# Optimization experiments

Measured on AMD Instinct MI355X. Metric: run time of the kernel, lower is better.

## Reference

```python
import jax, jax.numpy as jnp
import numpy as np

B, L, E, H = 1, 2048, 1024, 16
HW = E // H  # head width = 64
SCALE = HW ** -0.5


def setup_inputs() -> dict:
    key = jax.random.key(0)
    ks = jax.random.split(key, 8)
    x = jax.random.normal(ks[0], (B, L, E), dtype=jnp.float32)
    mask = jax.random.bernoulli(ks[1], 0.9, (B, L))
    mask = mask.at[:, 0].set(True)  # guarantee at least one valid key per batch
    bias = jax.random.normal(ks[2], (B, L, L, H), dtype=jnp.float32)
    # torch nn.Linear stores weight as [out, in]; we keep that convention
    w_proj = jax.random.normal(ks[3], (3 * E, E), dtype=jnp.float32) * (E ** -0.5)
    w_o = jax.random.normal(ks[4], (E, E), dtype=jnp.float32) * (E ** -0.5)
    b_o = jax.random.normal(ks[5], (E,), dtype=jnp.float32) * 0.02
    w_g = jax.random.normal(ks[6], (E, E), dtype=jnp.float32) * (E ** -0.5)
    b_g = jax.random.normal(ks[7], (E,), dtype=jnp.float32) * 0.02
    return {"x": x, "mask": mask, "bias": bias, "w_proj": w_proj,
            "w_o": w_o, "b_o": b_o, "w_g": w_g, "b_g": b_g}


def reference(x, mask, bias, w_proj, w_o, b_o, w_g, b_g):
    # proj -> [B, L, 3E], rearrange '(h c)' with h=H so each head slice holds [q|k|v]
    t = jnp.einsum('ble,fe->blf', x, w_proj)               # [B, L, 3E]
    t = t.reshape(B, L, H, 3 * HW).transpose(0, 2, 1, 3)   # [B, H, L, 3*HW]
    q, k, v = jnp.split(t, 3, axis=-1)                     # each [B, H, L, HW]
    a = jnp.einsum('bhqc,bhkc->bhqk', SCALE * q, k)        # [B, H, L, L]
    a = a + bias.transpose(0, 3, 1, 2)                     # bias: [B,Lq,Lk,H] -> [B,H,Lq,Lk]
    a = jnp.where(mask[:, None, None, :], a, -jnp.inf)
    a = jax.nn.softmax(a, axis=-1)
    y = jnp.einsum('bhqk,bhkc->bqhc', a, v).reshape(B, L, E)
    g = jax.nn.sigmoid(jnp.einsum('ble,fe->blf', x, w_g) + b_g)
    y = g * y
    return jnp.einsum('ble,fe->blf', y, w_o) + b_o
```

## Files before the change

kernel.cpp:

```cpp
#include <hip/hip_runtime.h>
#include <stdint.h>

#define LSEQ 2048
#define EMB  1024
#define NH   16
#define HWID 64
#define SCALEF 0.125f

typedef __attribute__((ext_vector_type(4))) float  f32x4;
typedef __attribute__((ext_vector_type(8))) short  bf16x8;
typedef __attribute__((ext_vector_type(8))) unsigned short u16x8;
typedef __attribute__((ext_vector_type(4))) unsigned short u16x4;

static __device__ __forceinline__ unsigned short f2bf(float f) {
    union { float f; unsigned int u; } v; v.f = f;
    unsigned int r = (v.u + 0x7FFFu + ((v.u >> 16) & 1u)) >> 16;
    return (unsigned short)r;
}
static __device__ __forceinline__ float bf2f(unsigned short h) {
    union { unsigned int u; float f; } v; v.u = ((unsigned int)h) << 16;
    return v.f;
}

static __device__ __forceinline__ void gload_lds16(const void* g, void* l) {
    __builtin_amdgcn_global_load_lds((const __attribute__((address_space(1))) void*)g,
                                     (__attribute__((address_space(3))) void*)l,
                                     16, 0, 0);
}

__global__ __launch_bounds__(256) void convert_kernel(
    const float* __restrict__ x, const float* __restrict__ wp,
    const float* __restrict__ wg, const float* __restrict__ wo,
    unsigned short* __restrict__ xb, unsigned short* __restrict__ wcat,
    unsigned short* __restrict__ wob)
{
    const int NX  = (LSEQ * EMB) / 4;
    const int NWP = (3 * EMB * EMB) / 4;
    const int NWG = (EMB * EMB) / 4;
    const int NWO = (EMB * EMB) / 4;
    const int total = NX + NWP + NWG + NWO;
    for (int i = blockIdx.x * blockDim.x + threadIdx.x; i < total;
         i += gridDim.x * blockDim.x) {
        const float4* src; unsigned short* dst; int j;
        if (i < NX)                  { src = (const float4*)x;  dst = xb;                  j = i; }
        else if (i < NX + NWP)       { src = (const float4*)wp; dst = wcat;                j = i - NX; }
        else if (i < NX + NWP + NWG) { src = (const float4*)wg; dst = wcat + 3 * EMB * EMB; j = i - NX - NWP; }
        else                         { src = (const float4*)wo; dst = wob;                 j = i - NX - NWP - NWG; }
        float4 v = src[j];
        u16x4 o;
        o.x = f2bf(v.x); o.y = f2bf(v.y); o.z = f2bf(v.z); o.w = f2bf(v.w);
        *(u16x4*)(dst + (size_t)j * 4) = o;
    }
}

__global__ void decode_mask_kernel(const unsigned char* __restrict__ mask,
                                   unsigned char* __restrict__ valid)
{
    __shared__ int cnt;
    if (threadIdx.x == 0) cnt = 0;
    __syncthreads();
    int c = 0;
    for (int i = threadIdx.x; i < LSEQ; i += 256) c += (mask[i] != 0);
    atomicAdd(&cnt, c);
    __syncthreads();
    bool isbyte = cnt > LSEQ / 2;
    for (int k = threadIdx.x; k < LSEQ; k += 256) {
        unsigned char v;
        if (isbyte) v = (mask[k] != 0);
        else        v = ((mask[4*k] | mask[4*k+1] | mask[4*k+2] | mask[4*k+3]) != 0);
        valid[k] = v;
    }
}

#define BM 128
#define BN 128
#define BK 64

__global__ __launch_bounds__(256) void gemm_bt_kernel(
    const unsigned short* __restrict__ A, const unsigned short* __restrict__ B,
    void* __restrict__ Cout, const float* __restrict__ biasN,
    int M, int N, int K, int epi)
{
    __shared__ unsigned short As[BM][BK];
    __shared__ unsigned short Bs[BN][BK];
    const int tid  = threadIdx.x;
    const int lane = tid & 63;
    const int w    = tid >> 6;
    const int wr   = w >> 1, wc = w & 1;
    const int row0 = blockIdx.y * BM;
    const int col0 = blockIdx.x * BN;
    const int lr = lane & 15;
    const int lg = lane >> 4;

    f32x4 acc[4][4];
    const f32x4 zf = {0.f, 0.f, 0.f, 0.f};
#pragma unroll
    for (int m = 0; m < 4; ++m)
#pragma unroll
        for (int n = 0; n < 4; ++n) acc[m][n] = zf;

    const char* Ab = (const char*)(A + (size_t)row0 * K);
    const char* Bb = (const char*)(B + (size_t)col0 * K);
    const int Kb = K * 2;

    for (int kt = 0; kt < K; kt += BK) {
#pragma unroll
        for (int i = 0; i < 4; ++i) {
            int o = (i * 256 + tid) * 16;
            int r = o >> 7, cb = o & 127;
            gload_lds16(Ab + (size_t)r * Kb + kt * 2 + cb, (char*)As + o);
        }
#pragma unroll
        for (int i = 0; i < 4; ++i) {
            int o = (i * 256 + tid) * 16;
            int r = o >> 7, cb = o & 127;
            gload_lds16(Bb + (size_t)r * Kb + kt * 2 + cb, (char*)Bs + o);
        }
        __syncthreads();
#pragma unroll
        for (int kk = 0; kk < 2; ++kk) {
            bf16x8 af[4], bfr[4];
            const int lk = kk * 32 + lg * 8;
#pragma unroll
            for (int m = 0; m < 4; ++m) af[m]  = *(const bf16x8*)&As[wr * 64 + m * 16 + lr][lk];
#pragma unroll
            for (int n = 0; n < 4; ++n) bfr[n] = *(const bf16x8*)&Bs[wc * 64 + n * 16 + lr][lk];
#pragma unroll
            for (int m = 0; m < 4; ++m)
#pragma unroll
                for (int n = 0; n < 4; ++n)
                    acc[m][n] = __builtin_amdgcn_mfma_f32_16x16x32_bf16(af[m], bfr[n], acc[m][n], 0, 0, 0);
        }
        __syncthreads();
    }

#pragma unroll
    for (int m = 0; m < 4; ++m)
#pragma unroll
        for (int n = 0; n < 4; ++n) {
            const int col = col0 + wc * 64 + n * 16 + lr;
#pragma unroll
            for (int r = 0; r < 4; ++r) {
                const int row = row0 + wr * 64 + m * 16 + lg * 4 + r;
                if (epi == 0)
                    ((unsigned short*)Cout)[(size_t)row * N + col] = f2bf(acc[m][n][r]);
                else
                    ((float*)Cout)[(size_t)row * N + col] = acc[m][n][r] + biasN[col];
            }
        }
}

__global__ __launch_bounds__(256) void rearrange_kernel(
    const unsigned short* __restrict__ T, const float* __restrict__ bg,
    unsigned short* __restrict__ Qh, unsigned short* __restrict__ Kh,
    unsigned short* __restrict__ G)
{
    const int l = blockIdx.x;
    const int t = threadIdx.x;
    const unsigned short* trow = T + (size_t)l * 4096;
    {
        const int tt = t & 127;
        const int h  = tt >> 3;
        const int c0 = (tt & 7) * 8;
        const bool isq = (t < 128);
        const int srcoff = h * 192 + (isq ? 0 : 64) + c0;
        u16x8 v = *(const u16x8*)(trow + srcoff);
        if (isq) {
#pragma unroll
            for (int j = 0; j < 8; ++j) v[j] = f2bf(bf2f(v[j]) * SCALEF);
        }
        unsigned short* dst = (isq ? Qh : Kh) + ((size_t)h * LSEQ + l) * HWID + c0;
        *(u16x8*)dst = v;
    }
    {
        const int f0 = t * 4;
        float4 b4 = *(const float4*)(bg + f0);
        u16x4 tv = *(const u16x4*)(trow + 3 * EMB + f0);
        u16x4 o;
        o.x = f2bf(1.f / (1.f + __expf(-(bf2f(tv.x) + b4.x))));
        o.y = f2bf(1.f / (1.f + __expf(-(bf2f(tv.y) + b4.y))));
        o.z = f2bf(1.f / (1.f + __expf(-(bf2f(tv.z) + b4.z))));
        o.w = f2bf(1.f / (1.f + __expf(-(bf2f(tv.w) + b4.w))));
        *(u16x4*)(G + (size_t)l * EMB + f0) = o;
    }
}

__global__ __launch_bounds__(256) void vtrans_kernel(
    const unsigned short* __restrict__ T, unsigned short* __restrict__ VT)
{
    __shared__ unsigned short tile[64][72];
    const int h  = blockIdx.x & 15;
    const int lt = blockIdx.x >> 4;
    const int l0 = lt * 64;
    const int t  = threadIdx.x;
    {
        const int i = t >> 2, c0 = (t & 3) * 16;
        const unsigned short* src = T + (size_t)(l0 + i) * 4096 + h * 192 + 128;
        *(u16x8*)&tile[i][c0]     = *(const u16x8*)(src + c0);
        *(u16x8*)&tile[i][c0 + 8] = *(const u16x8*)(src + c0 + 8);
    }
    __syncthreads();
    {
        const int c = t >> 2, j0 = (t & 3) * 16;
        unsigned short* dst = VT + ((size_t)h * HWID + c) * LSEQ + l0 + j0;
        u16x8 a, b;
#pragma unroll
        for (int j = 0; j < 8; ++j) a[j] = tile[j0 + j][c];
#pragma unroll
        for (int j = 0; j < 8; ++j) b[j] = tile[j0 + 8 + j][c];
        *(u16x8*)dst       = a;
        *(u16x8*)(dst + 8) = b;
    }
}

#define NT 32
#define SLOT 32768

__global__ __launch_bounds__(512, 4) void attn_kernel(
    const unsigned short* __restrict__ Qh, const unsigned short* __restrict__ Kh,
    const unsigned short* __restrict__ VT, const float* __restrict__ bias,
    const unsigned char* __restrict__ valid,
    float* __restrict__ Op, float* __restrict__ Ml)
{
    __shared__ char ring[2][SLOT];
    __shared__ unsigned short ps[8][16][40];
    __shared__ unsigned char vld[LSEQ];

    const int tid  = threadIdx.x;
    const int lane = tid & 63;
    const int w    = tid >> 6;
    const int bi = blockIdx.x;
    const int hg = bi >> 7;
    const int u  = bi & 127;
    const int qt = u >> 1;
    const int sp = u & 1;
    const int h4 = hg * 4;
    const int h    = h4 + (w & 3);
    const int q0b  = qt * 32;
    const int q0w  = q0b + (w >> 2) * 16;
    const int koff = sp * 1024;
    const int lr   = lane & 15;
    const int lg   = lane >> 4;
    const int hloc = w & 3;
    const int qloc = (w >> 2) * 16 + lg * 4;

    const unsigned short* Qbase = Qh + ((size_t)h * LSEQ + q0w) * HWID;
    const bf16x8 qa0 = *(const bf16x8*)(Qbase + lr * HWID + lg * 8);
    const bf16x8 qa1 = *(const bf16x8*)(Qbase + lr * HWID + 32 + lg * 8);

    const unsigned short* Vbase = VT + (size_t)h * HWID * LSEQ;
    const char* bias_base = (const char*)bias;
    const unsigned short* Khb = Kh;

    {
        uchar4 m4 = *(const uchar4*)(valid + tid * 4);
        *(uchar4*)(vld + tid * 4) = m4;
    }
    __syncthreads();

    auto stage = [&](int t) {
        char* base = ring[t & 1];
        const int kg = koff + t * 32;
#pragma unroll
        for (int p2 = 0; p2 < 2; ++p2) {
            const int jj = p2 * 512 + tid;
            const int q = jj >> 5, k = jj & 31;
            gload_lds16(bias_base + (((size_t)(q0b + q) * LSEQ + kg + k) * NH + h4) * 4,
                        base + jj * 16);
        }
#pragma unroll
        for (int p2 = 0; p2 < 2; ++p2) {
            const int jj = p2 * 512 + tid;
            const int hl = jj >> 8, k = (jj >> 3) & 31, c4 = jj & 7;
            gload_lds16(Khb + ((size_t)(h4 + hl) * LSEQ + kg + k) * HWID + ((c4 ^ (k & 7)) * 8),
                        base + 16384 + jj * 16);
        }
    };

    float mrow[4], lrow[4];
    f32x4 acc[4];
    const f32x4 zf = {0.f, 0.f, 0.f, 0.f};
#pragma unroll
    for (int r = 0; r < 4; ++r) { mrow[r] = -1e30f; lrow[r] = 0.f; }
#pragma unroll
    for (int c = 0; c < 4; ++c) acc[c] = zf;

    stage(0);
    stage(1);
    bf16x8 vb_cur[4], vb_nxt[4];
#pragma unroll
    for (int ct = 0; ct < 4; ++ct)
        vb_cur[ct] = *(const bf16x8*)(Vbase + (size_t)(ct * 16 + lr) * LSEQ + koff + lg * 8);

    for (int t = 0; t < NT; ++t) {
        asm volatile("s_waitcnt vmcnt(8)" ::: "memory");
        __builtin_amdgcn_s_barrier();
        asm volatile("" ::: "memory");

        const char* base = ring[t & 1];
        const int kg = koff + t * 32;
        const int kx = lr & 7;

        const unsigned short* klds = (const unsigned short*)(base + 16384);
        bf16x8 kb[2][2];
#pragma unroll
        for (int t2 = 0; t2 < 2; ++t2) {
            const int krow = (hloc * 32 + t2 * 16 + lr) * HWID;
            kb[t2][0] = *(const bf16x8*)(klds + krow + ((lg ^ kx) * 8));
            kb[t2][1] = *(const bf16x8*)(klds + krow + (((lg + 4) ^ kx) * 8));
        }

        f32x4 S[2];
#pragma unroll
        for (int t2 = 0; t2 < 2; ++t2) {
            f32x4 s = zf;
            s = __builtin_amdgcn_mfma_f32_16x16x32_bf16(qa0, kb[t2][0], s, 0, 0, 0);
            s = __builtin_amdgcn_mfma_f32_16x16x32_bf16(qa1, kb[t2][1], s, 0, 0, 0);
            S[t2] = s;
        }

        {
            const int kgn = koff + (t + 1 < NT ? t + 1 : t) * 32;
#pragma unroll
            for (int ct = 0; ct < 4; ++ct)
                vb_nxt[ct] = *(const bf16x8*)(Vbase + (size_t)(ct * 16 + lr) * LSEQ + kgn + lg * 8);
        }

        const bool v0 = vld[kg + lr] != 0;
        const bool v1 = vld[kg + 16 + lr] != 0;

        const float* bsf = (const float*)base;
        float sc[2][4], rm[4];
#pragma unroll
        for (int r = 0; r < 4; ++r) {
            const float b0 = bsf[((qloc + r) * 32 + lr) * 4 + hloc];
            const float b1 = bsf[((qloc + r) * 32 + 16 + lr) * 4 + hloc];
            sc[0][r] = v0 ? (S[0][r] + b0) : -1e30f;
            sc[1][r] = v1 ? (S[1][r] + b1) : -1e30f;
            rm[r] = fmaxf(sc[0][r], sc[1][r]);
        }
#pragma unroll
        for (int off = 1; off < 16; off <<= 1)
#pragma unroll
            for (int r = 0; r < 4; ++r)
                rm[r] = fmaxf(rm[r], __shfl_xor(rm[r], off, 64));

        const float need = fmaxf(fmaxf(rm[0] - mrow[0], rm[1] - mrow[1]),
                                 fmaxf(rm[2] - mrow[2], rm[3] - mrow[3]));
        if (!__all(need <= 8.0f)) {
            float sf[4];
#pragma unroll
            for (int r = 0; r < 4; ++r) {
                const float mn = fmaxf(mrow[r], rm[r]);
                sf[r] = __expf(mrow[r] - mn);
                mrow[r] = mn;
                lrow[r] *= sf[r];
            }
#pragma unroll
            for (int ct = 0; ct < 4; ++ct)
#pragma unroll
                for (int r = 0; r < 4; ++r) acc[ct][r] *= sf[r];
        }

        float rs[4], p0[4], p1[4];
#pragma unroll
        for (int r = 0; r < 4; ++r) {
            p0[r] = v0 ? __expf(sc[0][r] - mrow[r]) : 0.f;
            p1[r] = v1 ? __expf(sc[1][r] - mrow[r]) : 0.f;
            rs[r] = p0[r] + p1[r];
        }
#pragma unroll
        for (int off = 1; off < 16; off <<= 1)
#pragma unroll
            for (int r = 0; r < 4; ++r)
                rs[r] += __shfl_xor(rs[r], off, 64);
#pragma unroll
        for (int r = 0; r < 4; ++r) lrow[r] += rs[r];

#pragma unroll
        for (int r = 0; r < 4; ++r) {
            ps[w][lg * 4 + r][lr]      = f2bf(p0[r]);
            ps[w][lg * 4 + r][16 + lr] = f2bf(p1[r]);
        }
        const bf16x8 pa = *(const bf16x8*)&ps[w][lr][lg * 8];

#pragma unroll
        for (int ct = 0; ct < 4; ++ct)
            acc[ct] = __builtin_amdgcn_mfma_f32_16x16x32_bf16(pa, vb_cur[ct], acc[ct], 0, 0, 0);

        asm volatile("" ::: "memory");
        __builtin_amdgcn_s_barrier();
        asm volatile("" ::: "memory");
        if (t + 2 <= NT) stage(t + 2 < NT ? t + 2 : NT - 1);

#pragma unroll
        for (int ct = 0; ct < 4; ++ct) vb_cur[ct] = vb_nxt[ct];
    }

    const size_t rowb = ((size_t)sp * NH + h) * LSEQ;
#pragma unroll
    for (int ct = 0; ct < 4; ++ct)
#pragma unroll
        for (int r = 0; r < 4; ++r) {
            const int q = q0w + lg * 4 + r;
            Op[(rowb + q) * HWID + ct * 16 + lr] = acc[ct][r];
        }
    if (lr == 0) {
#pragma unroll
        for (int r = 0; r < 4; ++r) {
            const int q = q0w + lg * 4 + r;
            Ml[(rowb + q) * 2 + 0] = mrow[r];
            Ml[(rowb + q) * 2 + 1] = lrow[r];
        }
    }
}

__global__ __launch_bounds__(256) void combine_kernel(
    const float* __restrict__ Op, const float* __restrict__ Ml,
    const unsigned short* __restrict__ G, unsigned short* __restrict__ Yb)
{
    const int t   = threadIdx.x;
    const int c   = t & 63;
    const int row = blockIdx.x * 4 + (t >> 6);
    const int h   = row >> 11;
    const int q   = row & (LSEQ - 1);
    const size_t r0 = (size_t)h * LSEQ + q;
    const size_t r1 = ((size_t)NH + h) * LSEQ + q;
    const float m0 = Ml[r0 * 2 + 0], l0 = Ml[r0 * 2 + 1];
    const float m1 = Ml[r1 * 2 + 0], l1 = Ml[r1 * 2 + 1];
    const float mx = fmaxf(m0, m1);
    const float a0 = __expf(m0 - mx), a1 = __expf(m1 - mx);
    const float inv = 1.f / (l0 * a0 + l1 * a1);
    const float o0 = Op[r0 * HWID + c];
    const float o1 = Op[r1 * HWID + c];
    const float y = (o0 * a0 + o1 * a1) * inv;
    const int e = h * HWID + c;
    const float g = bf2f(G[(size_t)q * EMB + e]);
    Yb[(size_t)q * EMB + e] = f2bf(y * g);
}

extern "C" void kernel_launch(void* const* d_in, const int* in_sizes, int n_in,
                              void* d_out, int out_size, void* d_ws, size_t ws_size,
                              hipStream_t stream) {
    const float*         x      = (const float*)d_in[0];
    const unsigned char* mask   = (const unsigned char*)d_in[1];
    const float*         bias   = (const float*)d_in[2];
    const float*         w_proj = (const float*)d_in[3];
    const float*         w_o    = (const float*)d_in[4];
    const float*         b_o    = (const float*)d_in[5];
    const float*         w_g    = (const float*)d_in[6];
    const float*         b_g    = (const float*)d_in[7];
    float* out = (float*)d_out;
    (void)in_sizes; (void)n_in; (void)out_size; (void)ws_size;

    char* p = (char*)d_ws;
    auto alloc = [&](size_t bytes) {
        char* r = p; p += (bytes + 255) & ~(size_t)255; return r;
    };
    unsigned short* xb    = (unsigned short*)alloc((size_t)LSEQ * EMB * 2);
    unsigned short* wcat  = (unsigned short*)alloc((size_t)4 * EMB * EMB * 2);
    unsigned short* wob   = (unsigned short*)alloc((size_t)EMB * EMB * 2);
    unsigned short* T     = (unsigned short*)alloc((size_t)LSEQ * 4096 * 2);
    unsigned short* Qh    = (unsigned short*)alloc((size_t)NH * LSEQ * HWID * 2);
    unsigned short* Kh    = (unsigned short*)alloc((size_t)NH * LSEQ * HWID * 2);
    unsigned short* VT    = (unsigned short*)alloc((size_t)NH * HWID * LSEQ * 2);
    unsigned short* G     = (unsigned short*)alloc((size_t)LSEQ * EMB * 2);
    unsigned short* Yb    = (unsigned short*)alloc((size_t)LSEQ * EMB * 2);
    unsigned char*  vmask = (unsigned char*)alloc(LSEQ);
    float*          Op    = (float*)alloc((size_t)2 * NH * LSEQ * HWID * 4);
    float*          Ml    = (float*)alloc((size_t)2 * NH * LSEQ * 2 * 4);

    convert_kernel<<<1024, 256, 0, stream>>>(x, w_proj, w_g, w_o, xb, wcat, wob);
    decode_mask_kernel<<<1, 256, 0, stream>>>(mask, vmask);
    gemm_bt_kernel<<<dim3(4096 / BN, LSEQ / BM), 256, 0, stream>>>(
        xb, wcat, (void*)T, nullptr, LSEQ, 4096, EMB, 0);
    rearrange_kernel<<<LSEQ, 256, 0, stream>>>(T, b_g, Qh, Kh, G);
    vtrans_kernel<<<NH * (LSEQ / 64), 256, 0, stream>>>(T, VT);
    attn_kernel<<<512, 512, 0, stream>>>(Qh, Kh, VT, bias, vmask, Op, Ml);
    combine_kernel<<<NH * LSEQ / 4, 256, 0, stream>>>(Op, Ml, G, Yb);
    gemm_bt_kernel<<<dim3(EMB / BN, LSEQ / BM), 256, 0, stream>>>(
        Yb, wob, (void*)out, b_o, LSEQ, EMB, EMB, 1);
}
```

Before: 244.4 us.

## Stage bias through registers into padded per-head LDS; reduce row max lazily; MFMA row-sum

Bias tiles are now loaded into registers and written to a padded, head-major LDS array instead of being copied directly into LDS. This avoids bank conflicts when each wave reads its head's bias. The per-iteration row-max shuffle reduction now runs only when a rescale is triggered, using a lane-local max for the check. The row sum is computed with an extra MFMA against a vector of ones, which removes the sum shuffle reduction. In exchange, the vmcnt/lgkmcnt pipelining becomes more complex, register pressure rises from the bias prefetch buffers, and the denominator is now summed from bf16-rounded probabilities.

```diff
diff --git a/kernel.cpp b/kernel.cpp
--- a/kernel.cpp
+++ b/kernel.cpp
@@ -214,7 +214,6 @@
 }
 
 #define NT 32
-#define SLOT 32768
 
 __global__ __launch_bounds__(512, 4) void attn_kernel(
     const unsigned short* __restrict__ Qh, const unsigned short* __restrict__ Kh,
@@ -222,7 +221,8 @@
     const unsigned char* __restrict__ valid,
     float* __restrict__ Op, float* __restrict__ Ml)
 {
-    __shared__ char ring[2][SLOT];
+    __shared__ float bias_lds[2][4][1056];
+    __shared__ char kring[2][16384];
     __shared__ unsigned short ps[8][16][40];
     __shared__ unsigned char vld[LSEQ];
 
@@ -252,56 +252,81 @@
     const char* bias_base = (const char*)bias;
     const unsigned short* Khb = Kh;
 
-    {
-        uchar4 m4 = *(const uchar4*)(valid + tid * 4);
-        *(uchar4*)(vld + tid * 4) = m4;
-    }
-    __syncthreads();
-
-    auto stage = [&](int t) {
-        char* base = ring[t & 1];
+    bf16x8 ones;
+#pragma unroll
+    for (int j2 = 0; j2 < 8; ++j2) ones[j2] = (short)0x3F80;
+
+    auto stageK = [&](int t) {
+        char* base = kring[t & 1];
         const int kg = koff + t * 32;
-#pragma unroll
-        for (int p2 = 0; p2 < 2; ++p2) {
-            const int jj = p2 * 512 + tid;
-            const int q = jj >> 5, k = jj & 31;
-            gload_lds16(bias_base + (((size_t)(q0b + q) * LSEQ + kg + k) * NH + h4) * 4,
-                        base + jj * 16);
-        }
 #pragma unroll
         for (int p2 = 0; p2 < 2; ++p2) {
             const int jj = p2 * 512 + tid;
             const int hl = jj >> 8, k = (jj >> 3) & 31, c4 = jj & 7;
             gload_lds16(Khb + ((size_t)(h4 + hl) * LSEQ + kg + k) * HWID + ((c4 ^ (k & 7)) * 8),
-                        base + 16384 + jj * 16);
+                        base + jj * 16);
         }
     };
-
-    float mrow[4], lrow[4];
-    f32x4 acc[4];
+    auto loadBias = [&](int t, float4* bv) {
+        const int kg = koff + t * 32;
+#pragma unroll
+        for (int p2 = 0; p2 < 2; ++p2) {
+            const int jj = p2 * 512 + tid;
+            const int q = jj >> 5, k = jj & 31;
+            bv[p2] = *(const float4*)(bias_base +
+                     (((size_t)(q0b + q) * LSEQ + kg + k) * NH + h4) * 4);
+        }
+    };
+    auto writeBias = [&](int t, const float4* bv) {
+        float (*dst)[1056] = bias_lds[t & 1];
+#pragma unroll
+        for (int p2 = 0; p2 < 2; ++p2) {
+            const int jj = p2 * 512 + tid;
+            const int q = jj >> 5, k = jj & 31;
+            const int idx = q * 33 + k;
+            dst[0][idx] = bv[p2].x;
+            dst[1][idx] = bv[p2].y;
+            dst[2][idx] = bv[p2].z;
+            dst[3][idx] = bv[p2].w;
+        }
+    };
+
+    float mrow[4];
+    f32x4 acc[4], lsum;
     const f32x4 zf = {0.f, 0.f, 0.f, 0.f};
 #pragma unroll
-    for (int r = 0; r < 4; ++r) { mrow[r] = -1e30f; lrow[r] = 0.f; }
+    for (int r = 0; r < 4; ++r) mrow[r] = -1e30f;
 #pragma unroll
     for (int c = 0; c < 4; ++c) acc[c] = zf;
-
-    stage(0);
-    stage(1);
+    lsum = zf;
+
+    stageK(0); stageK(1);
+    float4 bw0[2], bwW[2], bwN[2];
+    loadBias(0, bw0);
+    loadBias(1, bwW);
     bf16x8 vb_cur[4], vb_nxt[4];
 #pragma unroll
     for (int ct = 0; ct < 4; ++ct)
         vb_cur[ct] = *(const bf16x8*)(Vbase + (size_t)(ct * 16 + lr) * LSEQ + koff + lg * 8);
-
+    {
+        uchar4 m4 = *(const uchar4*)(valid + tid * 4);
+        *(uchar4*)(vld + tid * 4) = m4;
+    }
+    __syncthreads();
+    writeBias(0, bw0);
+    asm volatile("s_waitcnt lgkmcnt(0)" ::: "memory");
+
+#pragma unroll 1
     for (int t = 0; t < NT; ++t) {
-        asm volatile("s_waitcnt vmcnt(8)" ::: "memory");
+        asm volatile("s_waitcnt vmcnt(4)" ::: "memory");
         __builtin_amdgcn_s_barrier();
         asm volatile("" ::: "memory");
 
-        const char* base = ring[t & 1];
+        const char* kbase = kring[t & 1];
         const int kg = koff + t * 32;
         const int kx = lr & 7;
 
-        const unsigned short* klds = (const unsigned short*)(base + 16384);
+        const unsigned short* klds = (const unsigned short*)kbase;
         bf16x8 kb[2][2];
 #pragma unroll
         for (int t2 = 0; t2 < 2; ++t2) {
@@ -319,8 +344,8 @@
             S[t2] = s;
         }
 
-        {
-            const int kgn = koff + (t + 1 < NT ? t + 1 : t) * 32;
+        if (t + 1 < NT) {
+            const int kgn = kg + 32;
 #pragma unroll
             for (int ct = 0; ct < 4; ++ct)
                 vb_nxt[ct] = *(const bf16x8*)(Vbase + (size_t)(ct * 16 + lr) * LSEQ + kgn + lg * 8);
@@ -329,53 +354,51 @@
         const bool v0 = vld[kg + lr] != 0;
         const bool v1 = vld[kg + 16 + lr] != 0;
 
-        const float* bsf = (const float*)base;
-        float sc[2][4], rm[4];
+        const float* bpl = bias_lds[t & 1][hloc];
+        float sc[2][4];
+        float lm[4];
 #pragma unroll
         for (int r = 0; r < 4; ++r) {
-            const float b0 = bsf[((qloc + r) * 32 + lr) * 4 + hloc];
-            const float b1 = bsf[((qloc + r) * 32 + 16 + lr) * 4 + hloc];
+            const int qrow = (qloc + r) * 33;
+            const float b0 = bpl[qrow + lr];
+            const float b1 = bpl[qrow + 16 + lr];
             sc[0][r] = v0 ? (S[0][r] + b0) : -1e30f;
             sc[1][r] = v1 ? (S[1][r] + b1) : -1e30f;
-            rm[r] = fmaxf(sc[0][r], sc[1][r]);
-        }
-#pragma unroll
-        for (int off = 1; off < 16; off <<= 1)
-#pragma unroll
-            for (int r = 0; r < 4; ++r)
-                rm[r] = fmaxf(rm[r], __shfl_xor(rm[r], off, 64));
-
-        const float need = fmaxf(fmaxf(rm[0] - mrow[0], rm[1] - mrow[1]),
-                                 fmaxf(rm[2] - mrow[2], rm[3] - mrow[3]));
+            lm[r] = fmaxf(sc[0][r], sc[1][r]);
+        }
+
+        const float need = fmaxf(fmaxf(lm[0] - mrow[0], lm[1] - mrow[1]),
+                                 fmaxf(lm[2] - mrow[2], lm[3] - mrow[3]));
         if (!__all(need <= 8.0f)) {
+            float rm[4];
+#pragma unroll
+            for (int r = 0; r < 4; ++r) rm[r] = lm[r];
+#pragma unroll
+            for (int off = 1; off < 16; off <<= 1)
+#pragma unroll
+                for (int r = 0; r < 4; ++r)
+                    rm[r] = fmaxf(rm[r], __shfl_xor(rm[r], off, 64));
             float sf[4];
 #pragma unroll
             for (int r = 0; r < 4; ++r) {
                 const float mn = fmaxf(mrow[r], rm[r]);
                 sf[r] = __expf(mrow[r] - mn);
                 mrow[r] = mn;
-                lrow[r] *= sf[r];
             }
 #pragma unroll
             for (int ct = 0; ct < 4; ++ct)
 #pragma unroll
                 for (int r = 0; r < 4; ++r) acc[ct][r] *= sf[r];
-        }
-
-        float rs[4], p0[4], p1[4];
+#pragma unroll
+            for (int r = 0; r < 4; ++r) lsum[r] *= sf[r];
+        }
+
+        float p0[4], p1[4];
 #pragma unroll
         for (int r = 0; r < 4; ++r) {
-            p0[r] = v0 ? __expf(sc[0][r] - mrow[r]) : 0.f;
-            p1[r] = v1 ? __expf(sc[1][r] - mrow[r]) : 0.f;
-            rs[r] = p0[r] + p1[r];
-        }
-#pragma unroll
-        for (int off = 1; off < 16; off <<= 1)
-#pragma unroll
-            for (int r = 0; r < 4; ++r)
-                rs[r] += __shfl_xor(rs[r], off, 64);
-#pragma unroll
-        for (int r = 0; r < 4; ++r) lrow[r] += rs[r];
+            p0[r] = __expf(sc[0][r] - mrow[r]);
+            p1[r] = __expf(sc[1][r] - mrow[r]);
+        }
 
 #pragma unroll
         for (int r = 0; r < 4; ++r) {
@@ -387,12 +410,22 @@
 #pragma unroll
         for (int ct = 0; ct < 4; ++ct)
             acc[ct] = __builtin_amdgcn_mfma_f32_16x16x32_bf16(pa, vb_cur[ct], acc[ct], 0, 0, 0);
-
-        asm volatile("" ::: "memory");
+        lsum = __builtin_amdgcn_mfma_f32_16x16x32_bf16(pa, ones, lsum, 0, 0, 0);
+
+        if (t + 1 < NT) {
+            asm volatile("s_waitcnt vmcnt(4)" ::: "memory");
+            writeBias(t + 1, bwW);
+        }
+        asm volatile("s_waitcnt lgkmcnt(0)" ::: "memory");
         __builtin_amdgcn_s_barrier();
         asm volatile("" ::: "memory");
-        if (t + 2 <= NT) stage(t + 2 < NT ? t + 2 : NT - 1);
-
+
+        if (t + 2 < NT) {
+            stageK(t + 2);
+            loadBias(t + 2, bwN);
+        }
+#pragma unroll
+        for (int p2 = 0; p2 < 2; ++p2) bwW[p2] = bwN[p2];
 #pragma unroll
         for (int ct = 0; ct < 4; ++ct) vb_cur[ct] = vb_nxt[ct];
     }
@@ -410,7 +443,7 @@
         for (int r = 0; r < 4; ++r) {
             const int q = q0w + lg * 4 + r;
             Ml[(rowb + q) * 2 + 0] = mrow[r];
-            Ml[(rowb + q) * 2 + 1] = lrow[r];
+            Ml[(rowb + q) * 2 + 1] = lsum[r];
         }
     }
 }
```

Result: faster. 234.9 us (-3.9%).
